# Kernel optimization log

Measured on AMD Instinct MI355X. Metric: run time of the kernel, lower is better.

The kernel has to match this reference:

```python
import math
import jax, jax.numpy as jnp
import numpy as np

B, C, T = 16, 64, 16384
KERNEL_LEN = 128
EPS = 1e-6


def setup_inputs() -> dict:
    key = jax.random.key(0)
    x = jax.random.normal(key, (B, C, T), dtype=jnp.float32)
    # learnable per-channel params at the torch init values
    log_alpha = jnp.full((C,), math.log(0.98 / (1.0 - 0.98)), dtype=jnp.float32)
    log_delta = jnp.full((C,), math.log(2.0), dtype=jnp.float32)
    log_root = jnp.full((C,), math.log(0.5), dtype=jnp.float32)
    log_s = jnp.full((C,), math.log(0.04 / (1.0 - 0.04)), dtype=jnp.float32)
    return {"x": x, "log_alpha": log_alpha, "log_delta": log_delta,
            "log_root": log_root, "log_s": log_s}


def _ema_kernel(log_s, L, dtype):
    # impulse[c, j] = s_c * (1 - s_c)^j, j = lag (0 = most recent)
    s = jax.nn.sigmoid(log_s).astype(dtype)  # (C,)
    j = jnp.arange(KERNEL_LEN, dtype=dtype)  # (Lk,)
    impulse = s[:, None] * (1.0 - s[:, None]) ** j[None, :]  # (C, Lk)
    impulse = impulse / (impulse.sum(axis=1, keepdims=True) + 1e-8)
    kernel = impulse[:, ::-1]              # causal conv: flip in time
    kernel = kernel[:, -L:]                # truncate if T < Lk
    return kernel[:, None, :]              # (C, 1, L) -> OIH for depthwise


def reference(x, log_alpha, log_delta, log_root, log_s):
    _, Cc, Tt = x.shape
    L = min(KERNEL_LEN, Tt)
    alpha = jax.nn.sigmoid(log_alpha)              # (C,)
    delta = jax.nn.softplus(log_delta) + 1e-6      # (C,)
    root = jax.nn.softplus(log_root) + 0.1         # (C,)

    x_mag = jnp.abs(x)                             # (B, C, T)
    kernel = _ema_kernel(log_s, L, x.dtype)        # (C, 1, L)
    x_pad = jnp.pad(x_mag, ((0, 0), (0, 0), (L - 1, 0)))  # causal left-pad
    M = jax.lax.conv_general_dilated(
        x_pad, kernel,
        window_strides=(1,), padding='VALID',
        dimension_numbers=('NCH', 'OIH', 'NCH'),
        feature_group_count=Cc)                     # (B, C, T) depthwise EMA

    alpha_bc = alpha[None, :, None]
    delta_bc = delta[None, :, None]
    root_bc = root[None, :, None]
    gain = (EPS + M) ** alpha_bc
    normed = x_mag / gain
    pcen = (normed + delta_bc) ** root_bc - delta_bc ** root_bc
    return pcen
```

## Files before the change

### kernel.cpp

```cpp
#include <hip/hip_runtime.h>
#include <math.h>

namespace {

constexpr int kT = 16384;
constexpr int kC = 64;
constexpr int kL = 128;
constexpr int kTileT = 4096;
constexpr int kThreads = 256;
constexpr int kChunk = kTileT / kThreads;
constexpr int kHaloChunks = kL / kChunk;
constexpr float kEps = 1e-6f;

__device__ __forceinline__ int pad4(int g) { return g + ((g >> 6) << 2); }

__device__ __forceinline__ float softplusf(float v) {
  return (v > 20.f) ? v : log1pf(expf(v));
}

__device__ __forceinline__ float fexp2(float v) { return __builtin_amdgcn_exp2f(v); }
__device__ __forceinline__ float flog2(float v) { return __builtin_amdgcn_logf(v); }

__global__ __launch_bounds__(kThreads, 8) void pcen_kernel(
    const float* __restrict__ x,
    const float* __restrict__ log_alpha,
    const float* __restrict__ log_delta,
    const float* __restrict__ log_root,
    const float* __restrict__ log_s,
    float* __restrict__ out)
{
  __shared__ alignas(16) float lds[4484];
  __shared__ float bsum[kHaloChunks + kThreads];

  const int tid  = threadIdx.x;
  const int row  = blockIdx.x >> 2;
  const int quad = blockIdx.x & 3;
  const int tb   = quad * kTileT;
  const int c    = row & (kC - 1);

  const float* __restrict__ xr   = x + (size_t)row * kT;
  float* __restrict__       outr = out + (size_t)row * kT;

  const float s    = 1.f / (1.f + expf(-log_s[c]));
  const float r    = 1.f - s;
  const float r2   = r * r;
  const float r4   = r2 * r2;
  const float r8   = r4 * r4;
  const float r16  = r8 * r8;
  const float r32  = r16 * r16;
  const float r64  = r32 * r32;
  const float r128 = r64 * r64;
  const float kn   = s / ((1.f - r128) + 1e-8f);
  const float alpha = 1.f / (1.f + expf(-log_alpha[c]));
  const float delta = softplusf(log_delta[c]) + 1e-6f;
  const float root  = softplusf(log_root[c]) + 0.1f;
  const float dr    = powf(delta, root);

  if (tid < kL / 4) {
    float4 v = make_float4(0.f, 0.f, 0.f, 0.f);
    if (tb) v = *(const float4*)(xr + tb - kL + 4 * tid);
    float4 a = make_float4(fabsf(v.x), fabsf(v.y), fabsf(v.z), fabsf(v.w));
    *(float4*)&lds[pad4(4 * tid)] = a;
  }
  #pragma unroll
  for (int it = 0; it < kTileT / 4 / kThreads; ++it) {
    const int m = it * kThreads + tid;
    const float4 v = *(const float4*)(xr + tb + 4 * m);
    float4 a = make_float4(fabsf(v.x), fabsf(v.y), fabsf(v.z), fabsf(v.w));
    *(float4*)&lds[pad4(kL + 4 * m)] = a;
  }
  __syncthreads();

  float xm[kChunk];
  const int lbase = kL + tid * kChunk;
  #pragma unroll
  for (int q = 0; q < kChunk / 4; ++q) {
    const float4 v = *(const float4*)&lds[pad4(lbase + 4 * q)];
    xm[4 * q + 0] = v.x; xm[4 * q + 1] = v.y;
    xm[4 * q + 2] = v.z; xm[4 * q + 3] = v.w;
  }
  float Bv = 0.f;
  #pragma unroll
  for (int k = 0; k < kChunk; ++k) Bv = fmaf(Bv, r, xm[k]);
  bsum[kHaloChunks + tid] = Bv;
  if (tid < kHaloChunks) {
    float Bh = 0.f;
    const int hbase = tid * kChunk;
    #pragma unroll
    for (int q = 0; q < kChunk / 4; ++q) {
      const float4 v = *(const float4*)&lds[pad4(hbase + 4 * q)];
      Bh = fmaf(Bh, r, v.x); Bh = fmaf(Bh, r, v.y);
      Bh = fmaf(Bh, r, v.z); Bh = fmaf(Bh, r, v.w);
    }
    bsum[tid] = Bh;
  }
  __syncthreads();

  float S = bsum[tid];
  #pragma unroll
  for (int m = 1; m < kHaloChunks; ++m) S = fmaf(S, r16, bsum[tid + m]);

  #pragma unroll
  for (int q = 0; q < kChunk / 4; ++q) {
    const float4 ov = *(const float4*)&lds[pad4(lbase - kL + 4 * q)];
    const float olds[4] = {ov.x, ov.y, ov.z, ov.w};
    #pragma unroll
    for (int j = 0; j < 4; ++j) {
      const int k = 4 * q + j;
      const float xv = xm[k];
      S = fmaf(S, r, xv);
      S = fmaf(-r128, olds[j], S);
      const float M      = kn * S;
      const float ginv   = fexp2(-alpha * flog2(kEps + M));
      const float normed = xv * ginv;
      xm[k] = fexp2(root * flog2(normed + delta)) - dr;
    }
  }
  __syncthreads();

  #pragma unroll
  for (int q = 0; q < kChunk / 4; ++q) {
    float4 v = make_float4(xm[4 * q + 0], xm[4 * q + 1],
                           xm[4 * q + 2], xm[4 * q + 3]);
    *(float4*)&lds[pad4(lbase + 4 * q)] = v;
  }
  __syncthreads();

  #pragma unroll
  for (int it = 0; it < kTileT / 4 / kThreads; ++it) {
    const int m = it * kThreads + tid;
    const float4 v = *(const float4*)&lds[pad4(kL + 4 * m)];
    *(float4*)(outr + tb + 4 * m) = v;
  }
}

}

extern "C" void kernel_launch(void* const* d_in, const int* in_sizes, int n_in,
                              void* d_out, int out_size, void* d_ws, size_t ws_size,
                              hipStream_t stream) {
  const float* x  = (const float*)d_in[0];
  const float* la = (const float*)d_in[1];
  const float* ld = (const float*)d_in[2];
  const float* lr = (const float*)d_in[3];
  const float* ls = (const float*)d_in[4];
  float* out = (float*)d_out;

  constexpr int rows = 16 * 64;
  constexpr int blocksPerRow = kT / kTileT;
  constexpr int grid = rows * blocksPerRow;

  hipLaunchKernelGGL(pcen_kernel, dim3(grid), dim3(kThreads), 0, stream,
                     x, la, ld, lr, ls, out);
}
```

Measured before the change: 30.17 us.

## Split each block's tile into two sub-tiles with register prefetch double buffering

Each block now handles its 4096-sample span as two 2048-sample sub-tiles held in two LDS buffers. The second sub-tile's global loads are issued into registers before the first sub-tile is computed. The first sub-tile's outputs are then written out before the second is processed. The aim is to overlap global memory latency with the EMA/PCEN math in a bandwidth-bound kernel. It also moves the abs() to compute time, replaces the sigmoid/softplus/pow parameter math with fast exp2/log2 intrinsics, and halves the per-thread chunk (r8 stride). The cost is extra barriers and slightly more LDS per block.

```diff
diff --git a/kernel.cpp b/kernel.cpp
--- a/kernel.cpp
+++ b/kernel.cpp
@@ -6,20 +6,32 @@
 constexpr int kT = 16384;
 constexpr int kC = 64;
 constexpr int kL = 128;
-constexpr int kTileT = 4096;
+constexpr int kSub = 2048;
+constexpr int kSpan = 2 * kSub;
 constexpr int kThreads = 256;
-constexpr int kChunk = kTileT / kThreads;
+constexpr int kChunk = kSub / kThreads;
 constexpr int kHaloChunks = kL / kChunk;
+constexpr int kBufF = 2312;
 constexpr float kEps = 1e-6f;
 
 __device__ __forceinline__ int pad4(int g) { return g + ((g >> 6) << 2); }
-
-__device__ __forceinline__ float softplusf(float v) {
-  return (v > 20.f) ? v : log1pf(expf(v));
-}
 
 __device__ __forceinline__ float fexp2(float v) { return __builtin_amdgcn_exp2f(v); }
 __device__ __forceinline__ float flog2(float v) { return __builtin_amdgcn_logf(v); }
+
+constexpr float kLog2e  = 1.4426950408889634f;
+constexpr float kRlog2e = 0.6931471805599453f;
+
+__device__ __forceinline__ float fsigmoid(float z) {
+  return 1.f / (1.f + fexp2(-z * kLog2e));
+}
+__device__ __forceinline__ float fsoftplus(float v) {
+  return flog2(1.f + fexp2(v * kLog2e)) * kRlog2e;
+}
+
+__device__ __forceinline__ float4 ld4g(const float* p) { return *(const float4*)p; }
+__device__ __forceinline__ float4 ld4s(const float* b, int g) { return *(const float4*)&b[g]; }
+__device__ __forceinline__ void st4s(float* b, int g, float4 v) { *(float4*)&b[g] = v; }
 
 __global__ __launch_bounds__(kThreads, 8) void pcen_kernel(
     const float* __restrict__ x,
@@ -29,19 +41,20 @@
     const float* __restrict__ log_s,
     float* __restrict__ out)
 {
-  __shared__ alignas(16) float lds[4484];
+  __shared__ alignas(16) float A[kBufF];
+  __shared__ alignas(16) float Bb[kBufF];
   __shared__ float bsum[kHaloChunks + kThreads];
 
-  const int tid  = threadIdx.x;
-  const int row  = blockIdx.x >> 2;
-  const int quad = blockIdx.x & 3;
-  const int tb   = quad * kTileT;
-  const int c    = row & (kC - 1);
+  const int tid = threadIdx.x;
+  const int row = blockIdx.x >> 2;
+  const int q   = blockIdx.x & 3;
+  const int tb  = q * kSpan;
+  const int c   = row & (kC - 1);
 
   const float* __restrict__ xr   = x + (size_t)row * kT;
   float* __restrict__       outr = out + (size_t)row * kT;
 
-  const float s    = 1.f / (1.f + expf(-log_s[c]));
+  const float s    = fsigmoid(log_s[c]);
   const float r    = 1.f - s;
   const float r2   = r * r;
   const float r4   = r2 * r2;
@@ -51,65 +64,63 @@
   const float r64  = r32 * r32;
   const float r128 = r64 * r64;
   const float kn   = s / ((1.f - r128) + 1e-8f);
-  const float alpha = 1.f / (1.f + expf(-log_alpha[c]));
-  const float delta = softplusf(log_delta[c]) + 1e-6f;
-  const float root  = softplusf(log_root[c]) + 0.1f;
-  const float dr    = powf(delta, root);
-
-  if (tid < kL / 4) {
-    float4 v = make_float4(0.f, 0.f, 0.f, 0.f);
-    if (tb) v = *(const float4*)(xr + tb - kL + 4 * tid);
-    float4 a = make_float4(fabsf(v.x), fabsf(v.y), fabsf(v.z), fabsf(v.w));
-    *(float4*)&lds[pad4(4 * tid)] = a;
-  }
-  #pragma unroll
-  for (int it = 0; it < kTileT / 4 / kThreads; ++it) {
-    const int m = it * kThreads + tid;
-    const float4 v = *(const float4*)(xr + tb + 4 * m);
-    float4 a = make_float4(fabsf(v.x), fabsf(v.y), fabsf(v.z), fabsf(v.w));
-    *(float4*)&lds[pad4(kL + 4 * m)] = a;
-  }
-  __syncthreads();
+  const float alpha = fsigmoid(log_alpha[c]);
+  const float delta = fsoftplus(log_delta[c]) + 1e-6f;
+  const float root  = fsoftplus(log_root[c]) + 0.1f;
+  const float dr    = fexp2(root * flog2(delta));
+
+  const int lbase = kL + tid * kChunk;
+
+  float4 h0 = make_float4(0.f, 0.f, 0.f, 0.f);
+  if (tid < kL / 4) { if (tb) h0 = ld4g(xr + tb - kL + 4 * tid); }
+  const float4 v0a = ld4g(xr + tb + 4 * tid);
+  const float4 v0b = ld4g(xr + tb + 1024 + 4 * tid);
+  if (tid < kL / 4) st4s(A, pad4(4 * tid), h0);
+  st4s(A, pad4(kL + 4 * tid), v0a);
+  st4s(A, pad4(kL + 1024 + 4 * tid), v0b);
+  __syncthreads();
+
+  float4 h1 = make_float4(0.f, 0.f, 0.f, 0.f);
+  if (tid < kL / 4) h1 = ld4g(xr + tb + kSub - kL + 4 * tid);
+  const float4 v1a = ld4g(xr + tb + kSub + 4 * tid);
+  const float4 v1b = ld4g(xr + tb + kSub + 1024 + 4 * tid);
 
   float xm[kChunk];
-  const int lbase = kL + tid * kChunk;
-  #pragma unroll
-  for (int q = 0; q < kChunk / 4; ++q) {
-    const float4 v = *(const float4*)&lds[pad4(lbase + 4 * q)];
-    xm[4 * q + 0] = v.x; xm[4 * q + 1] = v.y;
-    xm[4 * q + 2] = v.z; xm[4 * q + 3] = v.w;
+  {
+    const float4 a0 = ld4s(A, pad4(lbase));
+    const float4 a1 = ld4s(A, pad4(lbase + 4));
+    xm[0]=a0.x; xm[1]=a0.y; xm[2]=a0.z; xm[3]=a0.w;
+    xm[4]=a1.x; xm[5]=a1.y; xm[6]=a1.z; xm[7]=a1.w;
   }
   float Bv = 0.f;
   #pragma unroll
-  for (int k = 0; k < kChunk; ++k) Bv = fmaf(Bv, r, xm[k]);
+  for (int k = 0; k < kChunk; ++k) Bv = fmaf(Bv, r, fabsf(xm[k]));
   bsum[kHaloChunks + tid] = Bv;
   if (tid < kHaloChunks) {
-    float Bh = 0.f;
-    const int hbase = tid * kChunk;
-    #pragma unroll
-    for (int q = 0; q < kChunk / 4; ++q) {
-      const float4 v = *(const float4*)&lds[pad4(hbase + 4 * q)];
-      Bh = fmaf(Bh, r, v.x); Bh = fmaf(Bh, r, v.y);
-      Bh = fmaf(Bh, r, v.z); Bh = fmaf(Bh, r, v.w);
-    }
+    const float4 ha = ld4s(A, pad4(tid * kChunk));
+    const float4 hb = ld4s(A, pad4(tid * kChunk + 4));
+    float Bh = fabsf(ha.x);
+    Bh = fmaf(Bh, r, fabsf(ha.y)); Bh = fmaf(Bh, r, fabsf(ha.z));
+    Bh = fmaf(Bh, r, fabsf(ha.w)); Bh = fmaf(Bh, r, fabsf(hb.x));
+    Bh = fmaf(Bh, r, fabsf(hb.y)); Bh = fmaf(Bh, r, fabsf(hb.z));
+    Bh = fmaf(Bh, r, fabsf(hb.w));
     bsum[tid] = Bh;
   }
   __syncthreads();
 
   float S = bsum[tid];
   #pragma unroll
-  for (int m = 1; m < kHaloChunks; ++m) S = fmaf(S, r16, bsum[tid + m]);
-
-  #pragma unroll
-  for (int q = 0; q < kChunk / 4; ++q) {
-    const float4 ov = *(const float4*)&lds[pad4(lbase - kL + 4 * q)];
+  for (int m = 1; m < kHaloChunks; ++m) S = fmaf(S, r8, bsum[tid + m]);
+  #pragma unroll
+  for (int q2 = 0; q2 < kChunk / 4; ++q2) {
+    const float4 ov = ld4s(A, pad4(tid * kChunk + 4 * q2));
     const float olds[4] = {ov.x, ov.y, ov.z, ov.w};
     #pragma unroll
     for (int j = 0; j < 4; ++j) {
-      const int k = 4 * q + j;
-      const float xv = xm[k];
+      const int k = 4 * q2 + j;
+      const float xv = fabsf(xm[k]);
       S = fmaf(S, r, xv);
-      S = fmaf(-r128, olds[j], S);
+      S = fmaf(-r128, fabsf(olds[j]), S);
       const float M      = kn * S;
       const float ginv   = fexp2(-alpha * flog2(kEps + M));
       const float normed = xv * ginv;
@@ -118,19 +129,70 @@
   }
   __syncthreads();
 
-  #pragma unroll
-  for (int q = 0; q < kChunk / 4; ++q) {
-    float4 v = make_float4(xm[4 * q + 0], xm[4 * q + 1],
-                           xm[4 * q + 2], xm[4 * q + 3]);
-    *(float4*)&lds[pad4(lbase + 4 * q)] = v;
-  }
-  __syncthreads();
-
-  #pragma unroll
-  for (int it = 0; it < kTileT / 4 / kThreads; ++it) {
-    const int m = it * kThreads + tid;
-    const float4 v = *(const float4*)&lds[pad4(kL + 4 * m)];
-    *(float4*)(outr + tb + 4 * m) = v;
+  if (tid < kL / 4) st4s(Bb, pad4(4 * tid), h1);
+  st4s(Bb, pad4(kL + 4 * tid), v1a);
+  st4s(Bb, pad4(kL + 1024 + 4 * tid), v1b);
+  st4s(A, pad4(lbase),     make_float4(xm[0], xm[1], xm[2], xm[3]));
+  st4s(A, pad4(lbase + 4), make_float4(xm[4], xm[5], xm[6], xm[7]));
+  __syncthreads();
+
+  {
+    const float4 o0 = ld4s(A, pad4(kL + 4 * tid));
+    const float4 o1 = ld4s(A, pad4(kL + 1024 + 4 * tid));
+    *(float4*)(outr + tb + 4 * tid) = o0;
+    *(float4*)(outr + tb + 1024 + 4 * tid) = o1;
+  }
+  {
+    const float4 a0 = ld4s(Bb, pad4(lbase));
+    const float4 a1 = ld4s(Bb, pad4(lbase + 4));
+    xm[0]=a0.x; xm[1]=a0.y; xm[2]=a0.z; xm[3]=a0.w;
+    xm[4]=a1.x; xm[5]=a1.y; xm[6]=a1.z; xm[7]=a1.w;
+  }
+  Bv = 0.f;
+  #pragma unroll
+  for (int k = 0; k < kChunk; ++k) Bv = fmaf(Bv, r, fabsf(xm[k]));
+  bsum[kHaloChunks + tid] = Bv;
+  if (tid < kHaloChunks) {
+    const float4 ha = ld4s(Bb, pad4(tid * kChunk));
+    const float4 hb = ld4s(Bb, pad4(tid * kChunk + 4));
+    float Bh = fabsf(ha.x);
+    Bh = fmaf(Bh, r, fabsf(ha.y)); Bh = fmaf(Bh, r, fabsf(ha.z));
+    Bh = fmaf(Bh, r, fabsf(ha.w)); Bh = fmaf(Bh, r, fabsf(hb.x));
+    Bh = fmaf(Bh, r, fabsf(hb.y)); Bh = fmaf(Bh, r, fabsf(hb.z));
+    Bh = fmaf(Bh, r, fabsf(hb.w));
+    bsum[tid] = Bh;
+  }
+  __syncthreads();
+
+  S = bsum[tid];
+  #pragma unroll
+  for (int m = 1; m < kHaloChunks; ++m) S = fmaf(S, r8, bsum[tid + m]);
+  #pragma unroll
+  for (int q2 = 0; q2 < kChunk / 4; ++q2) {
+    const float4 ov = ld4s(Bb, pad4(tid * kChunk + 4 * q2));
+    const float olds[4] = {ov.x, ov.y, ov.z, ov.w};
+    #pragma unroll
+    for (int j = 0; j < 4; ++j) {
+      const int k = 4 * q2 + j;
+      const float xv = fabsf(xm[k]);
+      S = fmaf(S, r, xv);
+      S = fmaf(-r128, fabsf(olds[j]), S);
+      const float M      = kn * S;
+      const float ginv   = fexp2(-alpha * flog2(kEps + M));
+      const float normed = xv * ginv;
+      xm[k] = fexp2(root * flog2(normed + delta)) - dr;
+    }
+  }
+  __syncthreads();
+
+  st4s(Bb, pad4(lbase),     make_float4(xm[0], xm[1], xm[2], xm[3]));
+  st4s(Bb, pad4(lbase + 4), make_float4(xm[4], xm[5], xm[6], xm[7]));
+  __syncthreads();
+  {
+    const float4 o0 = ld4s(Bb, pad4(kL + 4 * tid));
+    const float4 o1 = ld4s(Bb, pad4(kL + 1024 + 4 * tid));
+    *(float4*)(outr + tb + kSub + 4 * tid) = o0;
+    *(float4*)(outr + tb + kSub + 1024 + 4 * tid) = o1;
   }
 }
 
@@ -147,7 +209,7 @@
   float* out = (float*)d_out;
 
   constexpr int rows = 16 * 64;
-  constexpr int blocksPerRow = kT / kTileT;
+  constexpr int blocksPerRow = kT / kSpan;
   constexpr int grid = rows * blocksPerRow;
 
   hipLaunchKernelGGL(pcen_kernel, dim3(grid), dim3(kThreads), 0, stream,
```

After: 26.43 us. 12.4% less time.
